# Optimization experiments

Measured on AMD Instinct MI355X. Metric: run time of the kernel, lower is better.

The kernel has to match this reference:

```python
import jax, jax.numpy as jnp
import numpy as np

B, N, E = 64, 1024, 16384   # graphs, nodes/graph, edges/graph
F, H, T, C = 128, 64, 10, 2 # input_dim, hid_dim, token_num, num_classes
INNER_PRUNE, CROSS_PRUNE = 0.3, 0.1
NEG_SLOPE = 0.01            # ProG act() defaults to leaky_relu


def setup_inputs() -> dict:
    key = jax.random.key(0)
    ks = jax.random.split(key, 8)
    x = jax.random.normal(ks[0], (B, N, F), jnp.float32)
    edge_src = jax.random.randint(ks[1], (B, E), 0, N, jnp.int32)
    edge_dst = jax.random.randint(ks[2], (B, E), 0, N, jnp.int32)
    # kaiming_uniform(leaky_relu, a=0.01, fan_in) for prompt tokens
    bound = float(np.sqrt(6.0 / ((1.0 + NEG_SLOPE ** 2) * F)))
    tokens = jax.random.uniform(ks[3], (T, F), jnp.float32, -bound, bound)

    def lin(k, fi, fo):
        b = 1.0 / np.sqrt(fi)
        k1, k2 = jax.random.split(k)
        return (jax.random.uniform(k1, (fi, fo), jnp.float32, -b, b),
                jax.random.uniform(k2, (fo,), jnp.float32, -b, b))

    W1, b1 = lin(ks[4], F, H)   # GCNConv 1
    W2, b2 = lin(ks[5], H, H)   # GCNConv 2
    Wa, ba = lin(ks[6], H, C)   # answering head
    return dict(x=x, tokens=tokens, W1=W1, b1=b1, W2=W2, b2=b2,
                Wa=Wa, ba=ba, edge_src=edge_src, edge_dst=edge_dst)


def reference(x, tokens, W1, b1, W2, b2, Wa, ba, edge_src, edge_dst):
    dt = x.dtype
    # --- HeavyPrompt: thresholded adjacency (edge existence only; PyG GCNConv
    # is called without edge_weight, so the sim values / edge_attr are unused)
    M_in = (jax.nn.sigmoid(tokens @ tokens.T) >= INNER_PRUNE).astype(dt)          # [T,T]
    M_cr = (jax.nn.sigmoid(jnp.einsum('tf,bnf->btn', tokens, x)) >= CROSS_PRUNE).astype(dt)  # [B,T,N], token->node

    # --- GCN normalization with self-loops (deg over targets)
    deg_tok = 1.0 + M_in.sum(0)                                                   # [T] (tokens only receive inner edges)
    offs = (jnp.arange(B, dtype=edge_dst.dtype) * N)[:, None]
    src_g = (edge_src + offs).reshape(-1)                                         # [B*E] global node ids
    dst_g = (edge_dst + offs).reshape(-1)
    in_deg = jax.ops.segment_sum(jnp.ones_like(dst_g, dt), dst_g, B * N).reshape(B, N)
    deg_node = 1.0 + in_deg + M_cr.sum(1)                                         # [B,N]
    inv_s_tok = jax.lax.rsqrt(deg_tok)
    inv_s_node = jax.lax.rsqrt(deg_node)
    inv_node_flat = inv_s_node.reshape(-1)
    norm_in = M_in * inv_s_tok[:, None] * inv_s_tok[None, :]                      # [T,T]
    ew = inv_node_flat[src_g] * inv_node_flat[dst_g]                              # per-edge 1/sqrt(di*dj)

    def gcn(ht, hn, W, b):
        # GCNConv: linear -> normalized aggregation (incl. self loop) -> +bias
        ht = ht @ W                                                               # [T,Fo] (token stream is graph-independent)
        hn = jnp.einsum('bnf,fo->bno', hn, W)                                     # [B,N,Fo]
        out_tok = norm_in @ ht + ht * (1.0 / deg_tok)[:, None] + b
        hn_flat = hn.reshape(B * N, -1)
        agg = jax.ops.segment_sum(hn_flat[src_g] * ew[:, None], dst_g, B * N).reshape(B, N, -1)
        cross = jnp.einsum('btn,to->bno', M_cr * inv_s_tok[None, :, None], ht) * inv_s_node[..., None]
        out_node = agg + cross + hn * (1.0 / deg_node)[..., None] + b
        return out_tok, out_node

    ht, hn = gcn(tokens, x, W1, b1)
    lrelu = lambda v: jnp.where(v >= 0, v, NEG_SLOPE * v)                         # act(); dropout is eval no-op
    ht, hn = lrelu(ht), lrelu(hn)
    ht, hn = gcn(ht, hn, W2, b2)                                                  # node_emb
    # global_mean_pool over each prompted graph (T tokens + N nodes)
    graph_emb = (ht.sum(0)[None, :] + hn.sum(1)) / (T + N)                        # [B,H]
    return jax.nn.softmax(graph_emb @ Wa + ba, axis=1)                            # answering
```

## Files before the change

kernel.cpp:

```cpp
#include <hip/hip_runtime.h>
#include <hip/hip_bf16.h>
#include <stdint.h>

#define B_ 64
#define N_ 1024
#define E_ 16384
#define F_ 128
#define H_ 64
#define T_ 10
#define BN (B_*N_)
#define BE (B_*E_)

#define TH_INNER (-0.84729786f)
#define TH_CROSS (-2.1972246f)

typedef __attribute__((ext_vector_type(8))) short short8;
typedef __attribute__((ext_vector_type(4))) float f32x4;

__device__ __forceinline__ float ld1(const void* p, int i, int bf) {
    if (bf) {
        uint16_t u = ((const uint16_t*)p)[i];
        return __uint_as_float(((uint32_t)u) << 16);
    }
    return ((const float*)p)[i];
}

__device__ __forceinline__ short to_bf(float x) {
    return (short)__bfloat16_as_ushort(__float2bfloat16(x));
}

__device__ __forceinline__ uint32_t pack_bf2(float lo, float hi) {
    uint32_t l = (uint32_t)__bfloat16_as_ushort(__float2bfloat16(lo));
    uint32_t h = (uint32_t)__bfloat16_as_ushort(__float2bfloat16(hi));
    return l | (h << 16);
}

__device__ __forceinline__ float bflo(uint32_t u) { return __uint_as_float(u << 16); }
__device__ __forceinline__ float bfhi(uint32_t u) { return __uint_as_float(u & 0xffff0000u); }

__global__ __launch_bounds__(1024) void k_count_prep(const int* __restrict__ dst,
                                                     int* __restrict__ cnt4,
                                                     const void* __restrict__ W1,
                                                     const void* __restrict__ W2,
                                                     const void* __restrict__ tokens,
                                                     int* __restrict__ flag,
                                                     short8* __restrict__ Bfr,
                                                     short8* __restrict__ Bfr2,
                                                     float* __restrict__ gsum,
                                                     uint32_t* __restrict__ y1pad,
                                                     uint32_t* __restrict__ y2pad) {
    __shared__ int lcnt[N_];
    int t = threadIdx.x;
    if (blockIdx.x >= 256) {
        uint32_t du = ((const uint32_t*)tokens)[t & 63];
        float dlo = __uint_as_float(du << 16);
        unsigned long long vote = __ballot(fabsf(dlo) <= 1.0f);
        int bf = (vote == ~0ull) ? 1 : 0;
        if (blockIdx.x == 256 && t == 0) *flag = bf;
        int f = (int)(blockIdx.x - 256) * 1024 + t;
        if (f < 1280) {
            int c = f / 320, rem = f % 320;
            int nt = rem / 64, lane = rem % 64;
            int q = lane >> 4, n = nt * 16 + (lane & 15);
            int k0 = c * 32 + q * 8;
            short8 v;
#pragma unroll
            for (int j = 0; j < 8; ++j) {
                int k = k0 + j;
                float x = 0.f;
                if (n < H_) x = ld1(W1, k * H_ + n, bf);
                else if (n < H_ + T_) x = ld1(tokens, (n - H_) * F_ + k, bf);
                v[j] = to_bf(x);
            }
            Bfr[f] = v;
        } else if (f < 1792) {
            int f2 = f - 1280;
            int c = f2 / 256, rem = f2 % 256;
            int nt = rem / 64, lane = rem % 64;
            int q = lane >> 4, n = nt * 16 + (lane & 15);
            int k0 = c * 32 + q * 8;
            short8 v;
#pragma unroll
            for (int j = 0; j < 8; ++j) v[j] = to_bf(ld1(W2, (k0 + j) * H_ + n, bf));
            Bfr2[f2] = v;
        }
        return;
    }
    int g = blockIdx.x & 63, c = blockIdx.x >> 6;
    lcnt[t] = 0;
    if (c == 0 && t < 64) gsum[g * 64 + t] = 0.f;
    if (blockIdx.x == 0) {
        if (t < 32) y1pad[t] = 0;
        else if (t < 64) y2pad[t - 32] = 0;
    }
    __syncthreads();
#pragma unroll
    for (int it = 0; it < 4; ++it)
        atomicAdd(&lcnt[dst[g * E_ + c * 4096 + it * 1024 + t]], 1);
    __syncthreads();
    cnt4[c * BN + g * N_ + t] = lcnt[t];
}

__global__ __launch_bounds__(1024) void k_scan_tok(const int* __restrict__ cnt4,
                                                   int* __restrict__ cnt,
                                                   int* __restrict__ offs,
                                                   int* __restrict__ base4,
                                                   const void* __restrict__ tokens,
                                                   const void* __restrict__ b1,
                                                   const void* __restrict__ b2,
                                                   const short8* __restrict__ Bfr,
                                                   const short8* __restrict__ Bfr2,
                                                   const int* __restrict__ flag,
                                                   uint32_t* __restrict__ y1,
                                                   uint32_t* __restrict__ y2,
                                                   float* __restrict__ tok_sum) {
    __shared__ int wsum[16];
    __shared__ float nm[T_ * 16];
    __shared__ float ist_s[16], idt_s[16];
    __shared__ float htbuf[T_ * 64];
    __shared__ float h1s[T_ * 64];
    int t = threadIdx.x;
    if (blockIdx.x < 64) {
        int g = blockIdx.x;
        int c0 = cnt4[0 * BN + g * N_ + t];
        int c1 = cnt4[1 * BN + g * N_ + t];
        int c2 = cnt4[2 * BN + g * N_ + t];
        int c3 = cnt4[3 * BN + g * N_ + t];
        int v = c0 + c1 + c2 + c3;
        int sc = v;
#pragma unroll
        for (int d = 1; d < 64; d <<= 1) {
            int u = __shfl_up(sc, d);
            if ((t & 63) >= d) sc += u;
        }
        if ((t & 63) == 63) wsum[t >> 6] = sc;
        __syncthreads();
        if (t < 16) {
            int wsc = wsum[t];
#pragma unroll
            for (int d = 1; d < 16; d <<= 1) {
                int u = __shfl_up(wsc, d);
                if (t >= d) wsc += u;
            }
            wsum[t] = wsc;
        }
        __syncthreads();
        int base = sc - v + ((t >= 64) ? wsum[(t >> 6) - 1] : 0);
        int o = g * E_ + base;
        cnt[g * N_ + t] = v;
        offs[g * N_ + t] = o;
        base4[0 * BN + g * N_ + t] = o;
        base4[1 * BN + g * N_ + t] = o + c0;
        base4[2 * BN + g * N_ + t] = o + c0 + c1;
        base4[3 * BN + g * N_ + t] = o + c0 + c1 + c2;
        return;
    }
    int bf = *flag;
    int l = t;
    bool act = (l < 64);
    int m = l & 15, q = (l & 63) >> 4;
    int mrow = (m < T_) ? m : (T_ - 1);
    f32x4 accM = {};
    f32x4 acc1[4] = {};
    float istc = 0.f, idtc = 0.f;
    if (act) {
        short8 afr[4];
        if (bf) {
            const short8* ar = (const short8*)((const uint16_t*)tokens + mrow * F_);
#pragma unroll
            for (int c = 0; c < 4; ++c) afr[c] = ar[c * 4 + q];
        } else {
            const float* ar = (const float*)tokens + mrow * F_;
#pragma unroll
            for (int c = 0; c < 4; ++c)
#pragma unroll
                for (int j = 0; j < 8; ++j) afr[c][j] = to_bf(ar[c * 32 + q * 8 + j]);
        }
#pragma unroll
        for (int c = 0; c < 4; ++c) {
            accM = __builtin_amdgcn_mfma_f32_16x16x32_bf16(afr[c], Bfr[(c * 5 + 4) * 64 + l], accM, 0, 0, 0);
#pragma unroll
            for (int nt = 0; nt < 4; ++nt)
                acc1[nt] = __builtin_amdgcn_mfma_f32_16x16x32_bf16(afr[c], Bfr[(c * 5 + nt) * 64 + l], acc1[nt], 0, 0, 0);
        }
        int ccnt = 0;
#pragma unroll
        for (int r = 0; r < 4; ++r) {
            int row = q * 4 + r;
            if (row < T_ && m < T_ && accM[r] >= TH_INNER) ccnt++;
        }
        ccnt += __shfl_xor(ccnt, 16);
        ccnt += __shfl_xor(ccnt, 32);
        float deg = 1.f + (float)ccnt;
        istc = 1.f / sqrtf(deg);
        idtc = 1.f / deg;
        if (q == 0 && m < T_) { ist_s[m] = istc; idt_s[m] = idtc; }
#pragma unroll
        for (int nt = 0; nt < 4; ++nt)
#pragma unroll
            for (int r = 0; r < 4; ++r) {
                int row = q * 4 + r;
                if (row < T_) htbuf[row * 64 + nt * 16 + m] = acc1[nt][r];
            }
    }
    __syncthreads();
    if (act && m < T_) {
#pragma unroll
        for (int r = 0; r < 4; ++r) {
            int row = q * 4 + r;
            if (row < T_)
                nm[row * 16 + m] = (accM[r] >= TH_INNER) ? ist_s[row] * istc : 0.f;
        }
    }
    __syncthreads();
    if (act) {
        float htc[T_];
#pragma unroll
        for (int s = 0; s < T_; ++s) htc[s] = htbuf[s * 64 + l];
        float b1f = ld1(b1, l, bf);
#pragma unroll
        for (int tt = 0; tt < T_; ++tt) {
            float a = htc[tt] * idt_s[tt] + b1f;
#pragma unroll
            for (int s = 0; s < T_; ++s) a += nm[tt * 16 + s] * htc[s];
            a = (a >= 0.f) ? a : 0.01f * a;
            h1s[tt * 64 + l] = a;
            float v = ist_s[tt] * htc[tt];
            float vh = __shfl(v, l + 1);
            if ((l & 1) == 0) y1[(size_t)(BN + 1 + tt) * 32 + (l >> 1)] = pack_bf2(v, vh);
        }
    }
    __syncthreads();
    if (act) {
        short8 a2fr[2];
#pragma unroll
        for (int c = 0; c < 2; ++c)
#pragma unroll
            for (int j = 0; j < 8; ++j) a2fr[c][j] = to_bf(h1s[mrow * 64 + c * 32 + q * 8 + j]);
        f32x4 acc2[4] = {};
#pragma unroll
        for (int nt = 0; nt < 4; ++nt)
#pragma unroll
            for (int c = 0; c < 2; ++c)
                acc2[nt] = __builtin_amdgcn_mfma_f32_16x16x32_bf16(a2fr[c], Bfr2[(c * 4 + nt) * 64 + l], acc2[nt], 0, 0, 0);
#pragma unroll
        for (int nt = 0; nt < 4; ++nt)
#pragma unroll
            for (int r = 0; r < 4; ++r) {
                int row = q * 4 + r;
                if (row < T_) htbuf[row * 64 + nt * 16 + m] = acc2[nt][r];
            }
    }
    __syncthreads();
    if (act) {
        float htc[T_];
#pragma unroll
        for (int s = 0; s < T_; ++s) htc[s] = htbuf[s * 64 + l];
        float b2f = ld1(b2, l, bf);
        float ts = 0.f;
#pragma unroll
        for (int tt = 0; tt < T_; ++tt) {
            float o = htc[tt] * idt_s[tt] + b2f;
#pragma unroll
            for (int s = 0; s < T_; ++s) o += nm[tt * 16 + s] * htc[s];
            ts += o;
            float v = ist_s[tt] * htc[tt];
            float vh = __shfl(v, l + 1);
            if ((l & 1) == 0) y2[(size_t)(BN + 1 + tt) * 32 + (l >> 1)] = pack_bf2(v, vh);
        }
        tok_sum[l] = ts;
    }
}

__global__ __launch_bounds__(1024) void k_scatter(const int* __restrict__ src,
                                                  const int* __restrict__ dst,
                                                  const int* __restrict__ base4,
                                                  int* __restrict__ bucket) {
    __shared__ int cur[N_];
    int t = threadIdx.x;
    int g = blockIdx.x & 63, c = blockIdx.x >> 6;
    cur[t] = base4[c * BN + g * N_ + t];
    __syncthreads();
#pragma unroll
    for (int it = 0; it < 4; ++it) {
        int i = g * E_ + c * 4096 + it * 1024 + t;
        int d = dst[i];
        int p = atomicAdd(&cur[d], 1);
        bucket[p] = g * N_ + src[i];
    }
}

__global__ __launch_bounds__(256) void k_node_mfma(const void* __restrict__ x,
                                                   const short8* __restrict__ Bfr,
                                                   const int* __restrict__ cnt,
                                                   const int* __restrict__ flag,
                                                   uint32_t* __restrict__ y1,
                                                   float* __restrict__ inv_s,
                                                   int* __restrict__ maskA) {
    int bf = *flag;
    int tid = threadIdx.x;
    int lane = tid & 63, wv = tid >> 6;
    int g = blockIdx.x & 63, c = blockIdx.x >> 6;
    int row0 = g * N_ + c * 64 + wv * 16;
    int m = lane & 15, q = lane >> 4;
    int row = row0 + m;
    short8 afr[4];
    if (bf) {
        const short8* ar = (const short8*)((const uint16_t*)x + (size_t)row * F_);
#pragma unroll
        for (int cc = 0; cc < 4; ++cc) afr[cc] = ar[cc * 4 + q];
    } else {
        const float* ar = (const float*)x + (size_t)row * F_;
#pragma unroll
        for (int cc = 0; cc < 4; ++cc)
#pragma unroll
            for (int j = 0; j < 8; ++j)
                afr[cc][j] = to_bf(ar[cc * 32 + q * 8 + j]);
    }
    f32x4 acc[5] = {};
#pragma unroll
    for (int nt = 0; nt < 5; ++nt)
#pragma unroll
        for (int cc = 0; cc < 4; ++cc) {
            short8 bfr = Bfr[(cc * 5 + nt) * 64 + lane];
            acc[nt] = __builtin_amdgcn_mfma_f32_16x16x32_bf16(afr[cc], bfr, acc[nt], 0, 0, 0);
        }
    unsigned long long bal[4];
#pragma unroll
    for (int r = 0; r < 4; ++r) {
        int pred = (m < T_) && (acc[4][r] >= TH_CROSS);
        bal[r] = __ballot(pred);
    }
    float isv[4];
#pragma unroll
    for (int r = 0; r < 4; ++r) {
        int node = row0 + q * 4 + r;
        int mk = (int)((bal[r] >> (q * 16)) & 0x3FF);
        int ec = cnt[node];
        int pc = __popc((unsigned)mk);
        float deg = 1.f + (float)ec + (float)pc;
        isv[r] = 1.f / sqrtf(deg);
        if (m == 0) { inv_s[node] = isv[r]; maskA[node] = mk; }
    }
#pragma unroll
    for (int r = 0; r < 4; ++r) {
        int node = row0 + q * 4 + r;
#pragma unroll
        for (int nt = 0; nt < 4; ++nt) {
            float v = acc[nt][r] * isv[r];
            float vh = __shfl(v, lane + 1);
            if ((m & 1) == 0)
                y1[(size_t)node * 32 + nt * 8 + (m >> 1)] = pack_bf2(v, vh);
        }
    }
}

#define NROWS (N_ + 12)

__device__ __forceinline__ void stage_slice(uint32_t* __restrict__ ys,
                                            const uint32_t* __restrict__ yg,
                                            const uint32_t* __restrict__ yall,
                                            int tid) {
#pragma unroll
    for (int it = 0; it < 9; ++it) {
        int idx = it * 1024 + tid;
        if (idx < NROWS * 8) {
            int r = idx >> 3, gg = idx & 7;
// ... 36 lines not shown
        uint4 u = *(const uint4*)&ys[(N_ + 1 + tk) * 32 + wp * 4];
        a[0] += bflo(u.x); a[1] += bfhi(u.x);
        a[2] += bflo(u.y); a[3] += bfhi(u.y);
        a[4] += bflo(u.z); a[5] += bfhi(u.z);
        a[6] += bflo(u.w); a[7] += bfhi(u.w);
    }
    {
        uint4 u = *(const uint4*)&ys[self_l * 32 + wp * 4];
        a[0] += bflo(u.x); a[1] += bfhi(u.x);
        a[2] += bflo(u.y); a[3] += bfhi(u.y);
        a[4] += bflo(u.z); a[5] += bfhi(u.z);
        a[6] += bflo(u.w); a[7] += bfhi(u.w);
    }
}

__global__ __launch_bounds__(1024, 1) void k_layer1(const uint32_t* __restrict__ y1,
                                                    const float* __restrict__ inv_s,
                                                    const int* __restrict__ cnt,
                                                    const int* __restrict__ offs,
                                                    const int* __restrict__ maskA,
                                                    const int* __restrict__ bucket,
                                                    const void* __restrict__ b1,
                                                    const short8* __restrict__ Bfr2,
                                                    const int* __restrict__ flag,
                                                    uint32_t* __restrict__ y2) {
    __shared__ uint32_t y1s[NROWS * 32];
    __shared__ uint32_t h1w[16][9 * 36];
    int bf = *flag;
    int tid = threadIdx.x;
    int lane = tid & 63, wv = tid >> 6;
    int gi = lane >> 3, wp = lane & 7;
    int g = blockIdx.x & 63, c = blockIdx.x >> 6;
    stage_slice(y1s, y1 + (size_t)g * N_ * 32, y1, tid);
    int nbase = g * N_ + c * 256 + wv * 16;
    int ln16 = lane & 15;
    int cntv = cnt[nbase + ln16];
    int offv = offs[nbase + ln16];
    float isvv = inv_s[nbase + ln16];
    int mskv = maskA[nbase + ln16];
    float bc[8];
#pragma unroll
    for (int j = 0; j < 8; ++j) bc[j] = ld1(b1, wp * 8 + j, bf);
    if (lane < 36) h1w[wv][8 * 36 + lane] = 0;
    __syncthreads();
    int m = lane & 15, q = lane >> 4;
    int mr = (m < 8) ? m : 8;
    for (int k = 0; k < 2; ++k) {
        int ni = k * 8 + gi;
        int cnt_g = __shfl(cntv, ni);
        int off_g = __shfl(offv, ni);
        int msk_g = __shfl(mskv, ni);
        float is_g = __shfl(isvv, ni);
        float a[8];
        gather_grp(y1s, bucket, cnt_g, off_g, msk_g, c * 256 + wv * 16 + ni, wp, a);
        uint32_t pk[4];
#pragma unroll
        for (int j = 0; j < 4; ++j) {
            float h0 = a[2 * j] * is_g + bc[2 * j];
            float h1v = a[2 * j + 1] * is_g + bc[2 * j + 1];
            h0 = (h0 >= 0.f) ? h0 : 0.01f * h0;
            h1v = (h1v >= 0.f) ? h1v : 0.01f * h1v;
            pk[j] = pack_bf2(h0, h1v);
        }
#pragma unroll
        for (int j = 0; j < 4; ++j) h1w[wv][gi * 36 + wp * 4 + j] = pk[j];
        short8 afr[2];
#pragma unroll
        for (int cc = 0; cc < 2; ++cc)
            afr[cc] = *(const short8*)&h1w[wv][mr * 36 + cc * 16 + q * 4];
        f32x4 acc[4] = {};
#pragma unroll
        for (int nt = 0; nt < 4; ++nt)
#pragma unroll
            for (int cc = 0; cc < 2; ++cc)
                acc[nt] = __builtin_amdgcn_mfma_f32_16x16x32_bf16(afr[cc], Bfr2[(cc * 4 + nt) * 64 + lane], acc[nt], 0, 0, 0);
#pragma unroll
        for (int r = 0; r < 4; ++r) {
            int tr = q * 4 + r;
            if (tr < 8) {
                int node = nbase + k * 8 + tr;
                float is = __shfl(isvv, k * 8 + tr);
#pragma unroll
                for (int nt = 0; nt < 4; ++nt) {
                    float v = acc[nt][r] * is;
                    float vh = __shfl(v, lane + 1);
                    if ((m & 1) == 0)
                        y2[(size_t)node * 32 + nt * 8 + (m >> 1)] = pack_bf2(v, vh);
                }
            }
        }
    }
}

__global__ __launch_bounds__(1024, 1) void k_layer2(const uint32_t* __restrict__ y2,
                                                    const float* __restrict__ inv_s,
                                                    const int* __restrict__ cnt,
                                                    const int* __restrict__ offs,
                                                    const int* __restrict__ maskA,
                                                    const int* __restrict__ bucket,
                                                    const void* __restrict__ b2,
                                                    const int* __restrict__ flag,
                                                    float* __restrict__ graph_sum) {
    __shared__ uint32_t y2s[NROWS * 32];
    __shared__ float pool[16][64];
    int bf = *flag;
    int tid = threadIdx.x;
    int lane = tid & 63, wv = tid >> 6;
    int gi = lane >> 3, wp = lane & 7;
    int g = blockIdx.x & 63, c = blockIdx.x >> 6;
    stage_slice(y2s, y2 + (size_t)g * N_ * 32, y2, tid);
    int nbase = g * N_ + c * 256 + wv * 16;
    int ln16 = lane & 15;
    int cntv = cnt[nbase + ln16];
    int offv = offs[nbase + ln16];
    float isvv = inv_s[nbase + ln16];
    int mskv = maskA[nbase + ln16];
    float bc[8];
#pragma unroll
    for (int j = 0; j < 8; ++j) bc[j] = ld1(b2, wp * 8 + j, bf);
    __syncthreads();
    float p[8];
#pragma unroll
    for (int j = 0; j < 8; ++j) p[j] = 0.f;
    for (int k = 0; k < 2; ++k) {
        int ni = k * 8 + gi;
        int cnt_g = __shfl(cntv, ni);
        int off_g = __shfl(offv, ni);
        int msk_g = __shfl(mskv, ni);
        float is_g = __shfl(isvv, ni);
        float a[8];
        gather_grp(y2s, bucket, cnt_g, off_g, msk_g, c * 256 + wv * 16 + ni, wp, a);
#pragma unroll
        for (int j = 0; j < 8; ++j) p[j] += a[j] * is_g + bc[j];
    }
#pragma unroll
    for (int j = 0; j < 8; ++j) {
        p[j] += __shfl_xor(p[j], 8);
        p[j] += __shfl_xor(p[j], 16);
        p[j] += __shfl_xor(p[j], 32);
    }
    if (gi == 0) {
#pragma unroll
        for (int j = 0; j < 8; ++j) pool[wv][wp * 8 + j] = p[j];
    }
    __syncthreads();
    if (tid < 64) {
        float s = 0.f;
#pragma unroll
        for (int w2 = 0; w2 < 16; ++w2) s += pool[w2][tid];
        atomicAdd(&graph_sum[g * H_ + tid], s);
    }
}

__global__ __launch_bounds__(64) void k_final(const float* __restrict__ graph_sum,
                                              const float* __restrict__ tok_sum,
                                              const void* __restrict__ Wa,
                                              const void* __restrict__ ba,
                                              const int* __restrict__ flag,
                                              void* __restrict__ out) {
    int bf = *flag;
    int b = blockIdx.x, l = threadIdx.x;
    float e = (tok_sum[l] + graph_sum[b * H_ + l]) * (1.0f / 1034.0f);
    float p0 = e * ld1(Wa, l * 2 + 0, bf);
    float p1 = e * ld1(Wa, l * 2 + 1, bf);
#pragma unroll
    for (int d = 32; d >= 1; d >>= 1) {
        p0 += __shfl_xor(p0, d);
        p1 += __shfl_xor(p1, d);
    }
    if (l == 0) {
        float l0 = p0 + ld1(ba, 0, bf);
        float l1 = p1 + ld1(ba, 1, bf);
        float mx = fmaxf(l0, l1);
        float e0 = expf(l0 - mx), e1 = expf(l1 - mx);
        float s = e0 + e1;
        float o0 = e0 / s, o1 = e1 / s;
        if (bf) {
            ((__hip_bfloat16*)out)[b * 2 + 0] = __float2bfloat16(o0);
            ((__hip_bfloat16*)out)[b * 2 + 1] = __float2bfloat16(o1);
        } else {
            ((float*)out)[b * 2 + 0] = o0;
            ((float*)out)[b * 2 + 1] = o1;
        }
    }
}

extern "C" void kernel_launch(void* const* d_in, const int* in_sizes, int n_in,
                              void* d_out, int out_size, void* d_ws, size_t ws_size,
                              hipStream_t stream) {
    (void)in_sizes; (void)n_in; (void)out_size; (void)ws_size;
    const void* x      = d_in[0];
    const void* tokens = d_in[1];
    const void* W1     = d_in[2];
    const void* b1     = d_in[3];
    const void* W2     = d_in[4];
    const void* b2     = d_in[5];
    const void* Wa     = d_in[6];
// ... 3 lines not shown

    char* w = (char*)d_ws;
    auto alloc = [&](size_t bytes) { void* p = (void*)w; w += (bytes + 255) & ~(size_t)255; return p; };
    int*      cnt       = (int*)alloc(BN * 4);
    int*      offs      = (int*)alloc(BN * 4);
    int*      maskA     = (int*)alloc(BN * 4);
    float*    inv_s     = (float*)alloc(BN * 4);
    int*      cnt4      = (int*)alloc((size_t)4 * BN * 4);
    int*      base4     = (int*)alloc((size_t)4 * BN * 4);
    int*      bucket    = (int*)alloc((size_t)BE * 4 + 512);
    uint32_t* y1        = (uint32_t*)alloc((size_t)(BN + 12) * 32 * 4);
    uint32_t* y2        = (uint32_t*)alloc((size_t)(BN + 12) * 32 * 4);
    float*    tok_sum   = (float*)alloc(H_ * 4);
    float*    graph_sum = (float*)alloc(B_ * H_ * 4);
    short8*   Bfr       = (short8*)alloc(4 * 5 * 64 * sizeof(short8));
    short8*   Bfr2      = (short8*)alloc(2 * 4 * 64 * sizeof(short8));
    int*      dflag     = (int*)alloc(256);

    k_count_prep<<<258, 1024, 0, stream>>>(edst, cnt4, W1, W2, tokens, dflag, Bfr, Bfr2,
                                           graph_sum, y1 + (size_t)BN * 32, y2 + (size_t)BN * 32);
    k_scan_tok  <<<65, 1024, 0, stream>>>(cnt4, cnt, offs, base4, tokens, b1, b2,
                                          Bfr, Bfr2, dflag, y1, y2, tok_sum);
    k_scatter   <<<256, 1024, 0, stream>>>(esrc, edst, base4, bucket);
    k_node_mfma <<<BN / 64, 256, 0, stream>>>(x, Bfr, cnt, dflag, y1, inv_s, maskA);
    k_layer1    <<<B_ * 4, 1024, 0, stream>>>(y1, inv_s, cnt, offs, maskA, bucket, b1, Bfr2, dflag, y2);
    k_layer2    <<<B_ * 4, 1024, 0, stream>>>(y2, inv_s, cnt, offs, maskA, bucket, b2, dflag, graph_sum);
    k_final     <<<B_, 64, 0, stream>>>(graph_sum, tok_sum, Wa, ba, dflag, d_out);
}
```

Before: 160.0 us.

## Fuse seven kernel launches into two cooperative kernels with grid syncs

Merges count/prep, scan/token, scatter and node MFMA into one cooperative kernel, and layer1, layer2 and final into a second, with grid.sync between phases. Destination indices stay in registers between counting and scattering, so they are not reloaded. The aim is to remove launch gaps and tail effects across many small kernels. In exchange, the whole grid waits at each barrier, and node MFMA work now runs with only 256 blocks of 1024 threads, which may lower parallelism compared with the old 1024-block launch.

Measured after the change: 585.5 us. 3.66x slower.

```diff
diff --git a/kernel.cpp b/kernel.cpp
--- a/kernel.cpp
+++ b/kernel.cpp
@@ -1,6 +1,9 @@
 #include <hip/hip_runtime.h>
 #include <hip/hip_bf16.h>
+#include <hip/hip_cooperative_groups.h>
 #include <stdint.h>
+
+namespace cg = cooperative_groups;
 
 #define B_ 64
 #define N_ 1024
@@ -38,94 +41,97 @@
 __device__ __forceinline__ float bflo(uint32_t u) { return __uint_as_float(u << 16); }
 __device__ __forceinline__ float bfhi(uint32_t u) { return __uint_as_float(u & 0xffff0000u); }
 
-__global__ __launch_bounds__(1024) void k_count_prep(const int* __restrict__ dst,
-                                                     int* __restrict__ cnt4,
-                                                     const void* __restrict__ W1,
-                                                     const void* __restrict__ W2,
-                                                     const void* __restrict__ tokens,
-                                                     int* __restrict__ flag,
-                                                     short8* __restrict__ Bfr,
-                                                     short8* __restrict__ Bfr2,
-                                                     float* __restrict__ gsum,
-                                                     uint32_t* __restrict__ y1pad,
-                                                     uint32_t* __restrict__ y2pad) {
-    __shared__ int lcnt[N_];
-    int t = threadIdx.x;
-    if (blockIdx.x >= 256) {
-        uint32_t du = ((const uint32_t*)tokens)[t & 63];
-        float dlo = __uint_as_float(du << 16);
-        unsigned long long vote = __ballot(fabsf(dlo) <= 1.0f);
-        int bf = (vote == ~0ull) ? 1 : 0;
-        if (blockIdx.x == 256 && t == 0) *flag = bf;
-        int f = (int)(blockIdx.x - 256) * 1024 + t;
-        if (f < 1280) {
-            int c = f / 320, rem = f % 320;
-            int nt = rem / 64, lane = rem % 64;
-            int q = lane >> 4, n = nt * 16 + (lane & 15);
-            int k0 = c * 32 + q * 8;
-            short8 v;
-#pragma unroll
-            for (int j = 0; j < 8; ++j) {
-                int k = k0 + j;
-                float x = 0.f;
-                if (n < H_) x = ld1(W1, k * H_ + n, bf);
-                else if (n < H_ + T_) x = ld1(tokens, (n - H_) * F_ + k, bf);
-                v[j] = to_bf(x);
-            }
-            Bfr[f] = v;
-        } else if (f < 1792) {
-            int f2 = f - 1280;
-            int c = f2 / 256, rem = f2 % 256;
-            int nt = rem / 64, lane = rem % 64;
-            int q = lane >> 4, n = nt * 16 + (lane & 15);
-            int k0 = c * 32 + q * 8;
-            short8 v;
-#pragma unroll
-            for (int j = 0; j < 8; ++j) v[j] = to_bf(ld1(W2, (k0 + j) * H_ + n, bf));
-            Bfr2[f2] = v;
-        }
-        return;
-    }
-    int g = blockIdx.x & 63, c = blockIdx.x >> 6;
-    lcnt[t] = 0;
-    if (c == 0 && t < 64) gsum[g * 64 + t] = 0.f;
-    if (blockIdx.x == 0) {
-        if (t < 32) y1pad[t] = 0;
-        else if (t < 64) y2pad[t - 32] = 0;
-    }
-    __syncthreads();
-#pragma unroll
-    for (int it = 0; it < 4; ++it)
-        atomicAdd(&lcnt[dst[g * E_ + c * 4096 + it * 1024 + t]], 1);
-    __syncthreads();
-    cnt4[c * BN + g * N_ + t] = lcnt[t];
-}
-
-__global__ __launch_bounds__(1024) void k_scan_tok(const int* __restrict__ cnt4,
-                                                   int* __restrict__ cnt,
-                                                   int* __restrict__ offs,
-                                                   int* __restrict__ base4,
-                                                   const void* __restrict__ tokens,
-                                                   const void* __restrict__ b1,
-                                                   const void* __restrict__ b2,
-                                                   const short8* __restrict__ Bfr,
-                                                   const short8* __restrict__ Bfr2,
-                                                   const int* __restrict__ flag,
-                                                   uint32_t* __restrict__ y1,
-                                                   uint32_t* __restrict__ y2,
-                                                   float* __restrict__ tok_sum) {
+__global__ __launch_bounds__(1024) void k_build(const int* __restrict__ src,
+                                                const int* __restrict__ dst,
+                                                int* __restrict__ cnt4,
+                                                int* __restrict__ base4,
+                                                int* __restrict__ cnt,
+                                                int* __restrict__ offs,
+                                                int* __restrict__ bucket,
+                                                const void* __restrict__ x,
+                                                const void* __restrict__ W1,
+                                                const void* __restrict__ W2,
+                                                const void* __restrict__ tokens,
+                                                const void* __restrict__ b1,
+                                                const void* __restrict__ b2,
+                                                int* __restrict__ flag,
+                                                short8* __restrict__ Bfr,
+                                                short8* __restrict__ Bfr2,
+                                                uint32_t* __restrict__ y1,
+                                                uint32_t* __restrict__ y2,
+                                                float* __restrict__ tok_sum,
+                                                float* __restrict__ inv_s,
+                                                int* __restrict__ maskA,
+                                                float* __restrict__ gsum) {
+    cg::grid_group grid = cg::this_grid();
+    __shared__ int lsh[N_];
     __shared__ int wsum[16];
     __shared__ float nm[T_ * 16];
     __shared__ float ist_s[16], idt_s[16];
     __shared__ float htbuf[T_ * 64];
     __shared__ float h1s[T_ * 64];
     int t = threadIdx.x;
-    if (blockIdx.x < 64) {
-        int g = blockIdx.x;
-        int c0 = cnt4[0 * BN + g * N_ + t];
-        int c1 = cnt4[1 * BN + g * N_ + t];
-        int c2 = cnt4[2 * BN + g * N_ + t];
-        int c3 = cnt4[3 * BN + g * N_ + t];
+    int bid = blockIdx.x;
+    int g = bid & 63, c = bid >> 6;
+
+    lsh[t] = 0;
+    if (c == 0 && t < 64) gsum[g * 64 + t] = 0.f;
+    if (bid == 0) {
+        if (t < 32) y1[(size_t)BN * 32 + t] = 0;
+        else if (t < 64) y2[(size_t)BN * 32 + (t - 32)] = 0;
+    }
+    __syncthreads();
+    int dval[4];
+#pragma unroll
+    for (int it = 0; it < 4; ++it) {
+        dval[it] = dst[g * E_ + c * 4096 + it * 1024 + t];
+        atomicAdd(&lsh[dval[it]], 1);
+    }
+    __syncthreads();
+    cnt4[c * BN + g * N_ + t] = lsh[t];
+    if (bid >= 254) {
+        uint32_t du = ((const uint32_t*)tokens)[t & 63];
+        float dlo = __uint_as_float(du << 16);
+        unsigned long long vote = __ballot(fabsf(dlo) <= 1.0f);
+        int bf = (vote == ~0ull) ? 1 : 0;
+        if (bid == 254 && t == 0) *flag = bf;
+        int f = (bid - 254) * 1024 + t;
+        if (f < 1280) {
+            int cc = f / 320, rem = f % 320;
+            int nt = rem / 64, lane = rem % 64;
+            int q = lane >> 4, n = nt * 16 + (lane & 15);
+            int k0 = cc * 32 + q * 8;
+            short8 v;
+#pragma unroll
+            for (int j = 0; j < 8; ++j) {
+                int k = k0 + j;
+                float xv = 0.f;
+                if (n < H_) xv = ld1(W1, k * H_ + n, bf);
+                else if (n < H_ + T_) xv = ld1(tokens, (n - H_) * F_ + k, bf);
+                v[j] = to_bf(xv);
+            }
+            Bfr[f] = v;
+        } else if (f < 1792) {
+            int f2 = f - 1280;
+            int cc = f2 / 256, rem = f2 % 256;
+            int nt = rem / 64, lane = rem % 64;
+            int q = lane >> 4, n = nt * 16 + (lane & 15);
+            int k0 = cc * 32 + q * 8;
+            short8 v;
+#pragma unroll
+            for (int j = 0; j < 8; ++j) v[j] = to_bf(ld1(W2, (k0 + j) * H_ + n, bf));
+            Bfr2[f2] = v;
+        }
+    }
+    __threadfence();
+    grid.sync();
+
+    if (bid < 64) {
+        int gg = bid;
+        int c0 = cnt4[0 * BN + gg * N_ + t];
+        int c1 = cnt4[1 * BN + gg * N_ + t];
+        int c2 = cnt4[2 * BN + gg * N_ + t];
+        int c3 = cnt4[3 * BN + gg * N_ + t];
         int v = c0 + c1 + c2 + c3;
         int sc = v;
 #pragma unroll
@@ -146,211 +152,196 @@
         }
         __syncthreads();
         int base = sc - v + ((t >= 64) ? wsum[(t >> 6) - 1] : 0);
-        int o = g * E_ + base;
-        cnt[g * N_ + t] = v;
-        offs[g * N_ + t] = o;
-        base4[0 * BN + g * N_ + t] = o;
-        base4[1 * BN + g * N_ + t] = o + c0;
-        base4[2 * BN + g * N_ + t] = o + c0 + c1;
-        base4[3 * BN + g * N_ + t] = o + c0 + c1 + c2;
-        return;
-    }
-    int bf = *flag;
-    int l = t;
-    bool act = (l < 64);
-    int m = l & 15, q = (l & 63) >> 4;
-    int mrow = (m < T_) ? m : (T_ - 1);
-    f32x4 accM = {};
-    f32x4 acc1[4] = {};
-    float istc = 0.f, idtc = 0.f;
-    if (act) {
+        int o = gg * E_ + base;
+        cnt[gg * N_ + t] = v;
+        offs[gg * N_ + t] = o;
+        base4[0 * BN + gg * N_ + t] = o;
+        base4[1 * BN + gg * N_ + t] = o + c0;
+        base4[2 * BN + gg * N_ + t] = o + c0 + c1;
+        base4[3 * BN + gg * N_ + t] = o + c0 + c1 + c2;
+    } else if (bid == 64) {
+        int bf = *flag;
+        int l = t;
+        bool act = (l < 64);
+        int m = l & 15, q = (l & 63) >> 4;
+        int mrow = (m < T_) ? m : (T_ - 1);
+        f32x4 accM = {};
+        f32x4 acc1[4] = {};
+        float istc = 0.f;
+        if (act) {
+            short8 afr[4];
+            if (bf) {
+                const short8* ar = (const short8*)((const uint16_t*)tokens + mrow * F_);
+#pragma unroll
+                for (int cc = 0; cc < 4; ++cc) afr[cc] = ar[cc * 4 + q];
+            } else {
+                const float* ar = (const float*)tokens + mrow * F_;
+#pragma unroll
+                for (int cc = 0; cc < 4; ++cc)
+#pragma unroll
+                    for (int j = 0; j < 8; ++j) afr[cc][j] = to_bf(ar[cc * 32 + q * 8 + j]);
+            }
+#pragma unroll
+            for (int cc = 0; cc < 4; ++cc) {
+                accM = __builtin_amdgcn_mfma_f32_16x16x32_bf16(afr[cc], Bfr[(cc * 5 + 4) * 64 + l], accM, 0, 0, 0);
+#pragma unroll
+                for (int nt = 0; nt < 4; ++nt)
+                    acc1[nt] = __builtin_amdgcn_mfma_f32_16x16x32_bf16(afr[cc], Bfr[(cc * 5 + nt) * 64 + l], acc1[nt], 0, 0, 0);
+            }
+            int ccnt = 0;
+#pragma unroll
+            for (int r = 0; r < 4; ++r) {
+                int row = q * 4 + r;
+                if (row < T_ && m < T_ && accM[r] >= TH_INNER) ccnt++;
+            }
+            ccnt += __shfl_xor(ccnt, 16);
+            ccnt += __shfl_xor(ccnt, 32);
+            float deg = 1.f + (float)ccnt;
+            istc = 1.f / sqrtf(deg);
+            if (q == 0 && m < T_) { ist_s[m] = istc; idt_s[m] = 1.f / deg; }
+#pragma unroll
+            for (int nt = 0; nt < 4; ++nt)
+#pragma unroll
+                for (int r = 0; r < 4; ++r) {
+                    int row = q * 4 + r;
+                    if (row < T_) htbuf[row * 64 + nt * 16 + m] = acc1[nt][r];
+                }
+        }
+        __syncthreads();
+        if (act && m < T_) {
+#pragma unroll
+            for (int r = 0; r < 4; ++r) {
+                int row = q * 4 + r;
+                if (row < T_)
+                    nm[row * 16 + m] = (accM[r] >= TH_INNER) ? ist_s[row] * istc : 0.f;
+            }
+        }
+        __syncthreads();
+        if (act) {
+            float htc[T_];
+#pragma unroll
+            for (int s = 0; s < T_; ++s) htc[s] = htbuf[s * 64 + l];
+            float b1f = ld1(b1, l, bf);
+#pragma unroll
+            for (int tt = 0; tt < T_; ++tt) {
+                float a = htc[tt] * idt_s[tt] + b1f;
+#pragma unroll
+                for (int s = 0; s < T_; ++s) a += nm[tt * 16 + s] * htc[s];
+                a = (a >= 0.f) ? a : 0.01f * a;
+                h1s[tt * 64 + l] = a;
+                float v = ist_s[tt] * htc[tt];
+                float vh = __shfl(v, l + 1);
+                if ((l & 1) == 0) y1[(size_t)(BN + 1 + tt) * 32 + (l >> 1)] = pack_bf2(v, vh);
+            }
+        }
+        __syncthreads();
+        if (act) {
+            short8 a2fr[2];
+#pragma unroll
+            for (int cc = 0; cc < 2; ++cc)
+#pragma unroll
+                for (int j = 0; j < 8; ++j) a2fr[cc][j] = to_bf(h1s[mrow * 64 + cc * 32 + q * 8 + j]);
+            f32x4 acc2[4] = {};
+#pragma unroll
+            for (int nt = 0; nt < 4; ++nt)
+#pragma unroll
+                for (int cc = 0; cc < 2; ++cc)
+                    acc2[nt] = __builtin_amdgcn_mfma_f32_16x16x32_bf16(a2fr[cc], Bfr2[(cc * 4 + nt) * 64 + l], acc2[nt], 0, 0, 0);
+#pragma unroll
+            for (int nt = 0; nt < 4; ++nt)
+#pragma unroll
+                for (int r = 0; r < 4; ++r) {
+                    int row = q * 4 + r;
+                    if (row < T_) htbuf[row * 64 + nt * 16 + m] = acc2[nt][r];
+                }
+        }
+        __syncthreads();
+        if (act) {
+            float htc[T_];
+#pragma unroll
+            for (int s = 0; s < T_; ++s) htc[s] = htbuf[s * 64 + l];
+            float b2f = ld1(b2, l, bf);
+            float ts = 0.f;
+#pragma unroll
+            for (int tt = 0; tt < T_; ++tt) {
+                float o = htc[tt] * idt_s[tt] + b2f;
+#pragma unroll
+                for (int s = 0; s < T_; ++s) o += nm[tt * 16 + s] * htc[s];
+                ts += o;
+                float v = ist_s[tt] * htc[tt];
+                float vh = __shfl(v, l + 1);
+                if ((l & 1) == 0) y2[(size_t)(BN + 1 + tt) * 32 + (l >> 1)] = pack_bf2(v, vh);
+            }
+            tok_sum[l] = ts;
+        }
+    }
+    __threadfence();
+    grid.sync();
+
+    lsh[t] = base4[c * BN + g * N_ + t];
+    __syncthreads();
+#pragma unroll
+    for (int it = 0; it < 4; ++it) {
+        int i = g * E_ + c * 4096 + it * 1024 + t;
+        int d = dval[it];
+        int p = atomicAdd(&lsh[d], 1);
+        bucket[p] = g * N_ + src[i];
+    }
+
+    {
+        int bf = *flag;
+        int lane = t & 63, w16 = t >> 6;
+        int row0 = g * N_ + c * 256 + w16 * 16;
+        int m = lane & 15, q = lane >> 4;
+        int row = row0 + m;
         short8 afr[4];
         if (bf) {
-            const short8* ar = (const short8*)((const uint16_t*)tokens + mrow * F_);
-#pragma unroll
-            for (int c = 0; c < 4; ++c) afr[c] = ar[c * 4 + q];
+            const short8* ar = (const short8*)((const uint16_t*)x + (size_t)row * F_);
+#pragma unroll
+            for (int cc = 0; cc < 4; ++cc) afr[cc] = ar[cc * 4 + q];
         } else {
-            const float* ar = (const float*)tokens + mrow * F_;
-#pragma unroll
-            for (int c = 0; c < 4; ++c)
-#pragma unroll
-                for (int j = 0; j < 8; ++j) afr[c][j] = to_bf(ar[c * 32 + q * 8 + j]);
-        }
-#pragma unroll
-        for (int c = 0; c < 4; ++c) {
-            accM = __builtin_amdgcn_mfma_f32_16x16x32_bf16(afr[c], Bfr[(c * 5 + 4) * 64 + l], accM, 0, 0, 0);
-#pragma unroll
-            for (int nt = 0; nt < 4; ++nt)
-                acc1[nt] = __builtin_amdgcn_mfma_f32_16x16x32_bf16(afr[c], Bfr[(c * 5 + nt) * 64 + l], acc1[nt], 0, 0, 0);
-        }
-        int ccnt = 0;
+            const float* ar = (const float*)x + (size_t)row * F_;
+#pragma unroll
+            for (int cc = 0; cc < 4; ++cc)
+#pragma unroll
+                for (int j = 0; j < 8; ++j)
+                    afr[cc][j] = to_bf(ar[cc * 32 + q * 8 + j]);
+        }
+        f32x4 acc[5] = {};
+#pragma unroll
+        for (int nt = 0; nt < 5; ++nt)
+#pragma unroll
+            for (int cc = 0; cc < 4; ++cc) {
+                short8 bfr = Bfr[(cc * 5 + nt) * 64 + lane];
+                acc[nt] = __builtin_amdgcn_mfma_f32_16x16x32_bf16(afr[cc], bfr, acc[nt], 0, 0, 0);
+            }
+        unsigned long long bal[4];
 #pragma unroll
         for (int r = 0; r < 4; ++r) {
-            int row = q * 4 + r;
-            if (row < T_ && m < T_ && accM[r] >= TH_INNER) ccnt++;
-        }
-        ccnt += __shfl_xor(ccnt, 16);
-        ccnt += __shfl_xor(ccnt, 32);
-        float deg = 1.f + (float)ccnt;
-        istc = 1.f / sqrtf(deg);
-        idtc = 1.f / deg;
-        if (q == 0 && m < T_) { ist_s[m] = istc; idt_s[m] = idtc; }
-#pragma unroll
-        for (int nt = 0; nt < 4; ++nt)
-#pragma unroll
-            for (int r = 0; r < 4; ++r) {
-                int row = q * 4 + r;
-                if (row < T_) htbuf[row * 64 + nt * 16 + m] = acc1[nt][r];
-            }
-    }
-    __syncthreads();
-    if (act && m < T_) {
+            int pred = (m < T_) && (acc[4][r] >= TH_CROSS);
+            bal[r] = __ballot(pred);
+        }
+        float isv[4];
 #pragma unroll
         for (int r = 0; r < 4; ++r) {
-            int row = q * 4 + r;
-            if (row < T_)
-                nm[row * 16 + m] = (accM[r] >= TH_INNER) ? ist_s[row] * istc : 0.f;
-        }
-    }
-    __syncthreads();
-    if (act) {
-        float htc[T_];
-#pragma unroll
-        for (int s = 0; s < T_; ++s) htc[s] = htbuf[s * 64 + l];
-        float b1f = ld1(b1, l, bf);
-#pragma unroll
-        for (int tt = 0; tt < T_; ++tt) {
-            float a = htc[tt] * idt_s[tt] + b1f;
-#pragma unroll
-            for (int s = 0; s < T_; ++s) a += nm[tt * 16 + s] * htc[s];
-            a = (a >= 0.f) ? a : 0.01f * a;
-            h1s[tt * 64 + l] = a;
-            float v = ist_s[tt] * htc[tt];
-            float vh = __shfl(v, l + 1);
-            if ((l & 1) == 0) y1[(size_t)(BN + 1 + tt) * 32 + (l >> 1)] = pack_bf2(v, vh);
-        }
-    }
-    __syncthreads();
-    if (act) {
-        short8 a2fr[2];
-#pragma unroll
-        for (int c = 0; c < 2; ++c)
-#pragma unroll
-            for (int j = 0; j < 8; ++j) a2fr[c][j] = to_bf(h1s[mrow * 64 + c * 32 + q * 8 + j]);
-        f32x4 acc2[4] = {};
-#pragma unroll
-        for (int nt = 0; nt < 4; ++nt)
-#pragma unroll
-            for (int c = 0; c < 2; ++c)
-                acc2[nt] = __builtin_amdgcn_mfma_f32_16x16x32_bf16(a2fr[c], Bfr2[(c * 4 + nt) * 64 + l], acc2[nt], 0, 0, 0);
-#pragma unroll
-        for (int nt = 0; nt < 4; ++nt)
-#pragma unroll
-            for (int r = 0; r < 4; ++r) {
-                int row = q * 4 + r;
-                if (row < T_) htbuf[row * 64 + nt * 16 + m] = acc2[nt][r];
-            }
-    }
-    __syncthreads();
-    if (act) {
-        float htc[T_];
-#pragma unroll
-        for (int s = 0; s < T_; ++s) htc[s] = htbuf[s * 64 + l];
-        float b2f = ld1(b2, l, bf);
-        float ts = 0.f;
-#pragma unroll
-        for (int tt = 0; tt < T_; ++tt) {
-            float o = htc[tt] * idt_s[tt] + b2f;
-#pragma unroll
-            for (int s = 0; s < T_; ++s) o += nm[tt * 16 + s] * htc[s];
-            ts += o;
-            float v = ist_s[tt] * htc[tt];
-            float vh = __shfl(v, l + 1);
-            if ((l & 1) == 0) y2[(size_t)(BN + 1 + tt) * 32 + (l >> 1)] = pack_bf2(v, vh);
-        }
-        tok_sum[l] = ts;
-    }
-}
-
-__global__ __launch_bounds__(1024) void k_scatter(const int* __restrict__ src,
-                                                  const int* __restrict__ dst,
-                                                  const int* __restrict__ base4,
-                                                  int* __restrict__ bucket) {
-    __shared__ int cur[N_];
-    int t = threadIdx.x;
-    int g = blockIdx.x & 63, c = blockIdx.x >> 6;
-    cur[t] = base4[c * BN + g * N_ + t];
-    __syncthreads();
-#pragma unroll
-    for (int it = 0; it < 4; ++it) {
-        int i = g * E_ + c * 4096 + it * 1024 + t;
-        int d = dst[i];
-        int p = atomicAdd(&cur[d], 1);
-        bucket[p] = g * N_ + src[i];
-    }
-}
-
-__global__ __launch_bounds__(256) void k_node_mfma(const void* __restrict__ x,
-                                                   const short8* __restrict__ Bfr,
-                                                   const int* __restrict__ cnt,
-                                                   const int* __restrict__ flag,
-                                                   uint32_t* __restrict__ y1,
-                                                   float* __restrict__ inv_s,
-                                                   int* __restrict__ maskA) {
-    int bf = *flag;
-    int tid = threadIdx.x;
-    int lane = tid & 63, wv = tid >> 6;
-    int g = blockIdx.x & 63, c = blockIdx.x >> 6;
-    int row0 = g * N_ + c * 64 + wv * 16;
-    int m = lane & 15, q = lane >> 4;
-    int row = row0 + m;
-    short8 afr[4];
-    if (bf) {
-        const short8* ar = (const short8*)((const uint16_t*)x + (size_t)row * F_);
-#pragma unroll
-        for (int cc = 0; cc < 4; ++cc) afr[cc] = ar[cc * 4 + q];
-    } else {
-        const float* ar = (const float*)x + (size_t)row * F_;
-#pragma unroll
-        for (int cc = 0; cc < 4; ++cc)
-#pragma unroll
-            for (int j = 0; j < 8; ++j)
-                afr[cc][j] = to_bf(ar[cc * 32 + q * 8 + j]);
-    }
-    f32x4 acc[5] = {};
-#pragma unroll
-    for (int nt = 0; nt < 5; ++nt)
-#pragma unroll
-        for (int cc = 0; cc < 4; ++cc) {
-            short8 bfr = Bfr[(cc * 5 + nt) * 64 + lane];
-            acc[nt] = __builtin_amdgcn_mfma_f32_16x16x32_bf16(afr[cc], bfr, acc[nt], 0, 0, 0);
-        }
-    unsigned long long bal[4];
-#pragma unroll
-    for (int r = 0; r < 4; ++r) {
-        int pred = (m < T_) && (acc[4][r] >= TH_CROSS);
-        bal[r] = __ballot(pred);
-    }
-    float isv[4];
-#pragma unroll
-    for (int r = 0; r < 4; ++r) {
-        int node = row0 + q * 4 + r;
-        int mk = (int)((bal[r] >> (q * 16)) & 0x3FF);
-        int ec = cnt[node];
-        int pc = __popc((unsigned)mk);
-        float deg = 1.f + (float)ec + (float)pc;
-        isv[r] = 1.f / sqrtf(deg);
-        if (m == 0) { inv_s[node] = isv[r]; maskA[node] = mk; }
-    }
-#pragma unroll
-    for (int r = 0; r < 4; ++r) {
-        int node = row0 + q * 4 + r;
-#pragma unroll
-        for (int nt = 0; nt < 4; ++nt) {
-            float v = acc[nt][r] * isv[r];
-            float vh = __shfl(v, lane + 1);
-            if ((m & 1) == 0)
-                y1[(size_t)node * 32 + nt * 8 + (m >> 1)] = pack_bf2(v, vh);
+            int node = row0 + q * 4 + r;
+            int mk = (int)((bal[r] >> (q * 16)) & 0x3FF);
+            int ec = cnt[node];
+            int pc = __popc((unsigned)mk);
+            float deg = 1.f + (float)ec + (float)pc;
+            isv[r] = 1.f / sqrtf(deg);
+            if (m == 0) { inv_s[node] = isv[r]; maskA[node] = mk; }
+        }
+#pragma unroll
+        for (int r = 0; r < 4; ++r) {
+            int node = row0 + q * 4 + r;
+#pragma unroll
+            for (int nt = 0; nt < 4; ++nt) {
+                float v = acc[nt][r] * isv[r];
+                float vh = __shfl(v, lane + 1);
+                if ((m & 1) == 0)
+                    y1[(size_t)node * 32 + nt * 8 + (m >> 1)] = pack_bf2(v, vh);
+            }
         }
     }
 }
@@ -417,173 +408,161 @@
     }
 }
 
-__global__ __launch_bounds__(1024, 1) void k_layer1(const uint32_t* __restrict__ y1,
-                                                    const float* __restrict__ inv_s,
-                                                    const int* __restrict__ cnt,
-                                                    const int* __restrict__ offs,
-                                                    const int* __restrict__ maskA,
-                                                    const int* __restrict__ bucket,
-                                                    const void* __restrict__ b1,
-                                                    const short8* __restrict__ Bfr2,
-                                                    const int* __restrict__ flag,
-                                                    uint32_t* __restrict__ y2) {
-    __shared__ uint32_t y1s[NROWS * 32];
-    __shared__ uint32_t h1w[16][9 * 36];
+__global__ __launch_bounds__(1024) void k_layers(const uint32_t* __restrict__ y1,
+                                                 uint32_t* __restrict__ y2,
+                                                 const float* __restrict__ inv_s,
+                                                 const int* __restrict__ cnt,
+                                                 const int* __restrict__ offs,
+                                                 const int* __restrict__ maskA,
+                                                 const int* __restrict__ bucket,
+                                                 const void* __restrict__ b1,
+                                                 const void* __restrict__ b2,
+                                                 const short8* __restrict__ Bfr2,
+                                                 const int* __restrict__ flag,
+                                                 float* __restrict__ graph_sum,
+                                                 const float* __restrict__ tok_sum,
+                                                 const void* __restrict__ Wa,
+                                                 const void* __restrict__ ba,
+                                                 void* __restrict__ out) {
+    cg::grid_group grid = cg::this_grid();
+    __shared__ uint32_t ysh[NROWS * 32];
+    __shared__ uint32_t aux[16 * 324];
     int bf = *flag;
     int tid = threadIdx.x;
     int lane = tid & 63, wv = tid >> 6;
     int gi = lane >> 3, wp = lane & 7;
     int g = blockIdx.x & 63, c = blockIdx.x >> 6;
-    stage_slice(y1s, y1 + (size_t)g * N_ * 32, y1, tid);
     int nbase = g * N_ + c * 256 + wv * 16;
     int ln16 = lane & 15;
     int cntv = cnt[nbase + ln16];
     int offv = offs[nbase + ln16];
     float isvv = inv_s[nbase + ln16];
     int mskv = maskA[nbase + ln16];
-    float bc[8];
-#pragma unroll
-    for (int j = 0; j < 8; ++j) bc[j] = ld1(b1, wp * 8 + j, bf);
-    if (lane < 36) h1w[wv][8 * 36 + lane] = 0;
-    __syncthreads();
     int m = lane & 15, q = lane >> 4;
     int mr = (m < 8) ? m : 8;
-    for (int k = 0; k < 2; ++k) {
-        int ni = k * 8 + gi;
-        int cnt_g = __shfl(cntv, ni);
-        int off_g = __shfl(offv, ni);
-        int msk_g = __shfl(mskv, ni);
-        float is_g = __shfl(isvv, ni);
-        float a[8];
-        gather_grp(y1s, bucket, cnt_g, off_g, msk_g, c * 256 + wv * 16 + ni, wp, a);
-        uint32_t pk[4];
-#pragma unroll
-        for (int j = 0; j < 4; ++j) {
-            float h0 = a[2 * j] * is_g + bc[2 * j];
-            float h1v = a[2 * j + 1] * is_g + bc[2 * j + 1];
-            h0 = (h0 >= 0.f) ? h0 : 0.01f * h0;
-            h1v = (h1v >= 0.f) ? h1v : 0.01f * h1v;
-            pk[j] = pack_bf2(h0, h1v);
-        }
-#pragma unroll
-        for (int j = 0; j < 4; ++j) h1w[wv][gi * 36 + wp * 4 + j] = pk[j];
-        short8 afr[2];
-#pragma unroll
-        for (int cc = 0; cc < 2; ++cc)
-            afr[cc] = *(const short8*)&h1w[wv][mr * 36 + cc * 16 + q * 4];
-        f32x4 acc[4] = {};
-#pragma unroll
-        for (int nt = 0; nt < 4; ++nt)
+
+    stage_slice(ysh, y1 + (size_t)g * N_ * 32, y1, tid);
+    {
+        float bc[8];
+#pragma unroll
+        for (int j = 0; j < 8; ++j) bc[j] = ld1(b1, wp * 8 + j, bf);
+        if (lane < 36) aux[wv * 324 + 8 * 36 + lane] = 0;
+        __syncthreads();
+        for (int k = 0; k < 2; ++k) {
+            int ni = k * 8 + gi;
+            int cnt_g = __shfl(cntv, ni);
+            int off_g = __shfl(offv, ni);
+            int msk_g = __shfl(mskv, ni);
+            float is_g = __shfl(isvv, ni);
+            float a[8];
+            gather_grp(ysh, bucket, cnt_g, off_g, msk_g, c * 256 + wv * 16 + ni, wp, a);
+            uint32_t pk[4];
+#pragma unroll
+            for (int j = 0; j < 4; ++j) {
+                float h0 = a[2 * j] * is_g + bc[2 * j];
+                float h1v = a[2 * j + 1] * is_g + bc[2 * j + 1];
+                h0 = (h0 >= 0.f) ? h0 : 0.01f * h0;
+                h1v = (h1v >= 0.f) ? h1v : 0.01f * h1v;
+                pk[j] = pack_bf2(h0, h1v);
+            }
+#pragma unroll
+            for (int j = 0; j < 4; ++j) aux[wv * 324 + gi * 36 + wp * 4 + j] = pk[j];
+            short8 afr[2];
 #pragma unroll
             for (int cc = 0; cc < 2; ++cc)
-                acc[nt] = __builtin_amdgcn_mfma_f32_16x16x32_bf16(afr[cc], Bfr2[(cc * 4 + nt) * 64 + lane], acc[nt], 0, 0, 0);
-#pragma unroll
-        for (int r = 0; r < 4; ++r) {
-            int tr = q * 4 + r;
-            if (tr < 8) {
-                int node = nbase + k * 8 + tr;
-                float is = __shfl(isvv, k * 8 + tr);
-#pragma unroll
-                for (int nt = 0; nt < 4; ++nt) {
-                    float v = acc[nt][r] * is;
-                    float vh = __shfl(v, lane + 1);
-                    if ((m & 1) == 0)
-                        y2[(size_t)node * 32 + nt * 8 + (m >> 1)] = pack_bf2(v, vh);
+                afr[cc] = *(const short8*)&aux[wv * 324 + mr * 36 + cc * 16 + q * 4];
+            f32x4 acc[4] = {};
+#pragma unroll
+            for (int nt = 0; nt < 4; ++nt)
+#pragma unroll
+                for (int cc = 0; cc < 2; ++cc)
+                    acc[nt] = __builtin_amdgcn_mfma_f32_16x16x32_bf16(afr[cc], Bfr2[(cc * 4 + nt) * 64 + lane], acc[nt], 0, 0, 0);
+#pragma unroll
+            for (int r = 0; r < 4; ++r) {
+                int tr = q * 4 + r;
+                if (tr < 8) {
+                    int node = nbase + k * 8 + tr;
+                    float is = __shfl(isvv, k * 8 + tr);
+#pragma unroll
+                    for (int nt = 0; nt < 4; ++nt) {
+                        float v = acc[nt][r] * is;
+                        float vh = __shfl(v, lane + 1);
+                        if ((m & 1) == 0)
+                            y2[(size_t)node * 32 + nt * 8 + (m >> 1)] = pack_bf2(v, vh);
+                    }
                 }
             }
         }
     }
-}
-
-__global__ __launch_bounds__(1024, 1) void k_layer2(const uint32_t* __restrict__ y2,
-                                                    const float* __restrict__ inv_s,
-                                                    const int* __restrict__ cnt,
-                                                    const int* __restrict__ offs,
-                                                    const int* __restrict__ maskA,
-                                                    const int* __restrict__ bucket,
-                                                    const void* __restrict__ b2,
-                                                    const int* __restrict__ flag,
-                                                    float* __restrict__ graph_sum) {
-    __shared__ uint32_t y2s[NROWS * 32];
-    __shared__ float pool[16][64];
-    int bf = *flag;
-    int tid = threadIdx.x;
-    int lane = tid & 63, wv = tid >> 6;
-    int gi = lane >> 3, wp = lane & 7;
-    int g = blockIdx.x & 63, c = blockIdx.x >> 6;
-    stage_slice(y2s, y2 + (size_t)g * N_ * 32, y2, tid);
-    int nbase = g * N_ + c * 256 + wv * 16;
-    int ln16 = lane & 15;
-    int cntv = cnt[nbase + ln16];
-    int offv = offs[nbase + ln16];
-    float isvv = inv_s[nbase + ln16];
-    int mskv = maskA[nbase + ln16];
-    float bc[8];
-#pragma unroll
-    for (int j = 0; j < 8; ++j) bc[j] = ld1(b2, wp * 8 + j, bf);
-    __syncthreads();
-    float p[8];
-#pragma unroll
-    for (int j = 0; j < 8; ++j) p[j] = 0.f;
-    for (int k = 0; k < 2; ++k) {
-        int ni = k * 8 + gi;
-        int cnt_g = __shfl(cntv, ni);
-        int off_g = __shfl(offv, ni);
-        int msk_g = __shfl(mskv, ni);
-        float is_g = __shfl(isvv, ni);
-        float a[8];
-        gather_grp(y2s, bucket, cnt_g, off_g, msk_g, c * 256 + wv * 16 + ni, wp, a);
-#pragma unroll
-        for (int j = 0; j < 8; ++j) p[j] += a[j] * is_g + bc[j];
-    }
-#pragma unroll
-    for (int j = 0; j < 8; ++j) {
-        p[j] += __shfl_xor(p[j], 8);
-        p[j] += __shfl_xor(p[j], 16);
-        p[j] += __shfl_xor(p[j], 32);
-    }
-    if (gi == 0) {
-#pragma unroll
-        for (int j = 0; j < 8; ++j) pool[wv][wp * 8 + j] = p[j];
-    }
-    __syncthreads();
-    if (tid < 64) {
-        float s = 0.f;
-#pragma unroll
-        for (int w2 = 0; w2 < 16; ++w2) s += pool[w2][tid];
-        atomicAdd(&graph_sum[g * H_ + tid], s);
-    }
-}
-
-__global__ __launch_bounds__(64) void k_final(const float* __restrict__ graph_sum,
-                                              const float* __restrict__ tok_sum,
-                                              const void* __restrict__ Wa,
-                                              const void* __restrict__ ba,
-                                              const int* __restrict__ flag,
-                                              void* __restrict__ out) {
-    int bf = *flag;
-    int b = blockIdx.x, l = threadIdx.x;
-    float e = (tok_sum[l] + graph_sum[b * H_ + l]) * (1.0f / 1034.0f);
-    float p0 = e * ld1(Wa, l * 2 + 0, bf);
-    float p1 = e * ld1(Wa, l * 2 + 1, bf);
-#pragma unroll
-    for (int d = 32; d >= 1; d >>= 1) {
-        p0 += __shfl_xor(p0, d);
-        p1 += __shfl_xor(p1, d);
-    }
-    if (l == 0) {
-        float l0 = p0 + ld1(ba, 0, bf);
-        float l1 = p1 + ld1(ba, 1, bf);
-        float mx = fmaxf(l0, l1);
-        float e0 = expf(l0 - mx), e1 = expf(l1 - mx);
-        float s = e0 + e1;
-        float o0 = e0 / s, o1 = e1 / s;
-        if (bf) {
-            ((__hip_bfloat16*)out)[b * 2 + 0] = __float2bfloat16(o0);
-            ((__hip_bfloat16*)out)[b * 2 + 1] = __float2bfloat16(o1);
-        } else {
-            ((float*)out)[b * 2 + 0] = o0;
-            ((float*)out)[b * 2 + 1] = o1;
+    __threadfence();
+    grid.sync();
+
+    stage_slice(ysh, y2 + (size_t)g * N_ * 32, y2, tid);
+    {
+        float* pool = (float*)aux;
+        float bc[8];
+#pragma unroll
+        for (int j = 0; j < 8; ++j) bc[j] = ld1(b2, wp * 8 + j, bf);
+        __syncthreads();
+        float p[8];
+#pragma unroll
+        for (int j = 0; j < 8; ++j) p[j] = 0.f;
+        for (int k = 0; k < 2; ++k) {
+            int ni = k * 8 + gi;
+            int cnt_g = __shfl(cntv, ni);
+            int off_g = __shfl(offv, ni);
+            int msk_g = __shfl(mskv, ni);
+            float is_g = __shfl(isvv, ni);
+            float a[8];
+            gather_grp(ysh, bucket, cnt_g, off_g, msk_g, c * 256 + wv * 16 + ni, wp, a);
+#pragma unroll
+            for (int j = 0; j < 8; ++j) p[j] += a[j] * is_g + bc[j];
+        }
+#pragma unroll
+        for (int j = 0; j < 8; ++j) {
+            p[j] += __shfl_xor(p[j], 8);
+            p[j] += __shfl_xor(p[j], 16);
+            p[j] += __shfl_xor(p[j], 32);
+        }
+        if (gi == 0) {
+#pragma unroll
+            for (int j = 0; j < 8; ++j) pool[wv * 64 + wp * 8 + j] = p[j];
+        }
+        __syncthreads();
+        if (tid < 64) {
+            float s = 0.f;
+#pragma unroll
+            for (int w2 = 0; w2 < 16; ++w2) s += pool[w2 * 64 + tid];
+            atomicAdd(&graph_sum[g * H_ + tid], s);
+        }
+    }
+    __threadfence();
+    grid.sync();
+
+    if (blockIdx.x < 64 && tid < 64) {
+        int b = blockIdx.x, l = tid;
+        float e = (tok_sum[l] + graph_sum[b * H_ + l]) * (1.0f / 1034.0f);
+        float p0 = e * ld1(Wa, l * 2 + 0, bf);
+        float p1 = e * ld1(Wa, l * 2 + 1, bf);
+#pragma unroll
+        for (int d = 32; d >= 1; d >>= 1) {
+            p0 += __shfl_xor(p0, d);
+            p1 += __shfl_xor(p1, d);
+        }
+        if (l == 0) {
+            float l0 = p0 + ld1(ba, 0, bf);
+            float l1 = p1 + ld1(ba, 1, bf);
+            float mx = fmaxf(l0, l1);
+            float e0 = expf(l0 - mx), e1 = expf(l1 - mx);
+            float s = e0 + e1;
+            float o0 = e0 / s, o1 = e1 / s;
+            if (bf) {
+                ((__hip_bfloat16*)out)[b * 2 + 0] = __float2bfloat16(o0);
+                ((__hip_bfloat16*)out)[b * 2 + 1] = __float2bfloat16(o1);
+            } else {
+                ((float*)out)[b * 2 + 0] = o0;
+                ((float*)out)[b * 2 + 1] = o1;
+            }
         }
     }
 }
@@ -617,16 +596,23 @@
     float*    tok_sum   = (float*)alloc(H_ * 4);
     float*    graph_sum = (float*)alloc(B_ * H_ * 4);
     short8*   Bfr       = (short8*)alloc(4 * 5 * 64 * sizeof(short8));
-    short8*   Bfr2      = (short8*)alloc(2 * 4 * 64 * sizeof(short8));
+    short8*   Bfr2     = (short8*)alloc(2 * 4 * 64 * sizeof(short8));
     int*      dflag     = (int*)alloc(256);
 
-    k_count_prep<<<258, 1024, 0, stream>>>(edst, cnt4, W1, W2, tokens, dflag, Bfr, Bfr2,
-                                           graph_sum, y1 + (size_t)BN * 32, y2 + (size_t)BN * 32);
-    k_scan_tok  <<<65, 1024, 0, stream>>>(cnt4, cnt, offs, base4, tokens, b1, b2,
-                                          Bfr, Bfr2, dflag, y1, y2, tok_sum);
-    k_scatter   <<<256, 1024, 0, stream>>>(esrc, edst, base4, bucket);
-    k_node_mfma <<<BN / 64, 256, 0, stream>>>(x, Bfr, cnt, dflag, y1, inv_s, maskA);
-    k_layer1    <<<B_ * 4, 1024, 0, stream>>>(y1, inv_s, cnt, offs, maskA, bucket, b1, Bfr2, dflag, y2);
-    k_layer2    <<<B_ * 4, 1024, 0, stream>>>(y2, inv_s, cnt, offs, maskA, bucket, b2, dflag, graph_sum);
-    k_final     <<<B_, 64, 0, stream>>>(graph_sum, tok_sum, Wa, ba, dflag, d_out);
-}
+    {
+        void* ka[] = { (void*)&esrc, (void*)&edst, (void*)&cnt4, (void*)&base4,
+                       (void*)&cnt, (void*)&offs, (void*)&bucket,
+                       (void*)&x, (void*)&W1, (void*)&W2, (void*)&tokens,
+                       (void*)&b1, (void*)&b2, (void*)&dflag, (void*)&Bfr, (void*)&Bfr2,
+                       (void*)&y1, (void*)&y2, (void*)&tok_sum,
+                       (void*)&inv_s, (void*)&maskA, (void*)&graph_sum };
+        hipLaunchCooperativeKernel((const void*)k_build, dim3(256), dim3(1024), ka, 0, stream);
+    }
+    {
+        void* ka[] = { (void*)&y1, (void*)&y2, (void*)&inv_s, (void*)&cnt, (void*)&offs,
+                       (void*)&maskA, (void*)&bucket, (void*)&b1, (void*)&b2,
+                       (void*)&Bfr2, (void*)&dflag, (void*)&graph_sum, (void*)&tok_sum,
+                       (void*)&Wa, (void*)&ba, (void*)&d_out };
+        hipLaunchCooperativeKernel((const void*)k_layers, dim3(256), dim3(1024), ka, 0, stream);
+    }
+}
```
